# Performance work log

Hardware: AMD Instinct MI355X
Metric: run time of the kernel (lower is better)

The kernel has to match this reference:

```python
import jax, jax.numpy as jnp
import numpy as np

TEMPERATURE = 0.05   # distiller.temperature
KD_WEIGHT = 1.0      # args.kd_weight
EPS = 1e-8
B, D = 128, 768


def _huber(diff):
    a = jnp.abs(diff)
    return jnp.where(a < 1.0, 0.5 * a * a, a - 0.5)


def _pairwise_sqdist(x):
    # ||xi||^2 + ||xj||^2 - 2 xi.xj  (squared euclidean, as in source)
    n2 = (x * x).sum(axis=1, keepdims=True)
    return n2 + n2.T - 2.0 * (x @ x.T)


def _distance_loss(s, t):
    ds = _pairwise_sqdist(s)          # [N,N]
    dt = _pairwise_sqdist(t)
    n = ds.shape[0]
    mask = jnp.triu(jnp.ones((n, n), bool), k=1)
    cnt = n * (n - 1) / 2.0
    mean_sd = jax.lax.stop_gradient(jnp.where(mask, ds, 0.0).sum() / cnt) + EPS
    mean_td = jnp.where(mask, dt, 0.0).sum() / cnt + EPS  # teacher is constant anyway
    loss = _huber(ds / mean_sd - dt / mean_td)
    return jnp.where(mask, loss, 0.0).sum() / cnt


def _angle_potentials(x):
    # diffs[i,j] = x[j] - x[i]; unit vectors; cos[i,j,k] = e[i,j] . e[k,j]
    diffs = x[None, :, :] - x[:, None, :]                       # [N,N,D]
    e = diffs / (jnp.linalg.norm(diffs, axis=-1, keepdims=True) + EPS)
    return jnp.einsum('ijd,kjd->ijk', e, e)                     # [N,N,N]


def _angle_loss(s, t):
    ps = _angle_potentials(s)
    pt = _angle_potentials(t)
    n = ps.shape[0]
    i = jnp.arange(n)
    # valid iff i != j, i != k, j != k  (matches the three masked diagonals)
    m = ((i[:, None, None] != i[None, :, None]) &
         (i[:, None, None] != i[None, None, :]) &
         (i[None, :, None] != i[None, None, :]))
    cnt = n * (n - 1) * (n - 2)
    return jnp.where(m, _huber(ps - pt), 0.0).sum() / cnt


def _contrastive_loss(sq, sp):
    scores = (sq @ sp.T) / TEMPERATURE                          # [B,B]
    tgt = jnp.arange(scores.shape[0])                           # * (B//B) == arange
    logZ = jax.nn.logsumexp(scores, axis=-1)
    return (logZ - jnp.take_along_axis(scores, tgt[:, None], axis=1)[:, 0]).mean()


def setup_inputs() -> dict:
    key = jax.random.key(0)
    k1, k2, k3, k4 = jax.random.split(key, 4)
    return {
        'student_qry': jax.random.normal(k1, (B, D), jnp.float32),
        'student_pos': jax.random.normal(k2, (B, D), jnp.float32),
        'teacher_qry': jax.random.normal(k3, (B, D), jnp.float32),
        'teacher_pos': jax.random.normal(k4, (B, D), jnp.float32),
    }


def reference(student_qry, student_pos, teacher_qry, teacher_pos):
    contrastive = _contrastive_loss(student_qry, student_pos)
    s = jnp.concatenate([student_qry, student_pos], axis=0)     # [2B,D]
    t = jnp.concatenate([teacher_qry, teacher_pos], axis=0)
    t = jax.lax.stop_gradient(t)                                # teacher under no_grad
    kd = 0.5 * _distance_loss(s, t) + 0.5 * _angle_loss(s, t)
    total = contrastive + KD_WEIGHT * kd
    return total, contrastive, kd
```

## Files before the change

kernel.cpp:

```cpp
#include <hip/hip_runtime.h>
#include <math.h>

#define N2   256
#define DIM  768
#define EPSF 1e-8f

#define OFF_PART  0u
#define OFF_PDIAG 1048576u
#define OFF_GS    1052672u
#define OFF_GT    1118208u
#define OFF_INVS  1183744u
#define OFF_INVT  1249280u
#define OFF_SLOT  1314816u
#define SL_DSDT 0
#define SL_CON  512
#define SL_ANG  640
#define SL_DIST 1152

__device__ inline float wave_reduce_sum(float v) {
    #pragma unroll
    for (int o = 32; o > 0; o >>= 1) v += __shfl_down(v, o, 64);
    return v;
}
__device__ inline float wave_reduce_max(float v) {
    #pragma unroll
    for (int o = 32; o > 0; o >>= 1) v = fmaxf(v, __shfl_down(v, o, 64));
    return v;
}
__device__ inline float block_reduce_sum(float v, volatile float* red) {
    float w = wave_reduce_sum(v);
    __syncthreads();
    if ((threadIdx.x & 63) == 0) red[threadIdx.x >> 6] = w;
    __syncthreads();
    return red[0] + red[1] + red[2] + red[3];
}
__device__ inline const float* rowptr(const float* q, const float* p, int r) {
    return (r < 128) ? (q + r * DIM) : (p + (r - 128) * DIM);
}

__global__ __launch_bounds__(256) void gemm_kernel(
        const float* __restrict__ sq, const float* __restrict__ sp,
        const float* __restrict__ tq, const float* __restrict__ tp,
        float* __restrict__ ws) {
    const int b = blockIdx.x, t = threadIdx.x;
    const int c = b & 7, mat = (b >> 3) & 1, tile = b >> 4;
    const int m0 = (tile >> 2) * 64, n0 = (tile & 3) * 64;
    const float* q = mat ? tq : sq;
    const float* p = mat ? tp : sp;

    __shared__ float As[64][100];
    __shared__ float Bs[64][100];

    const int srow = t >> 2, skq = (t & 3) * 4;
    const int kb = c * 96;
    const float* arow = rowptr(q, p, m0 + srow);
    const float* brow = rowptr(q, p, n0 + srow);
    #pragma unroll
    for (int m = 0; m < 6; ++m) {
        *(float4*)&As[srow][skq + 16 * m] = *(const float4*)&arow[kb + skq + 16 * m];
        *(float4*)&Bs[srow][skq + 16 * m] = *(const float4*)&brow[kb + skq + 16 * m];
    }
    __syncthreads();

    const int ty = t >> 4, tx = t & 15;
    float acc[4][4] = {};
    for (int k = 0; k < 96; k += 4) {
        float4 av[4], bv[4];
        #pragma unroll
        for (int r = 0; r < 4; ++r) av[r] = *(const float4*)&As[ty + 16 * r][k];
        #pragma unroll
        for (int cc = 0; cc < 4; ++cc) bv[cc] = *(const float4*)&Bs[tx + 16 * cc][k];
        #pragma unroll
        for (int r = 0; r < 4; ++r) {
            const float ar4[4] = {av[r].x, av[r].y, av[r].z, av[r].w};
            #pragma unroll
            for (int cc = 0; cc < 4; ++cc) {
                const float bc4[4] = {bv[cc].x, bv[cc].y, bv[cc].z, bv[cc].w};
                acc[r][cc] = fmaf(ar4[0], bc4[0], acc[r][cc]);
                acc[r][cc] = fmaf(ar4[1], bc4[1], acc[r][cc]);
                acc[r][cc] = fmaf(ar4[2], bc4[2], acc[r][cc]);
                acc[r][cc] = fmaf(ar4[3], bc4[3], acc[r][cc]);
            }
        }
    }
    float* P = ws + OFF_PART + (unsigned)(c * 2 + mat) * 65536u;
    #pragma unroll
    for (int r = 0; r < 4; ++r) {
        const int row = m0 + ty + 16 * r;
        #pragma unroll
        for (int cc = 0; cc < 4; ++cc)
            P[row * 256 + n0 + tx + 16 * cc] = acc[r][cc];
    }
    if (m0 == n0 && ty == tx) {
        float* PD = ws + OFF_PDIAG + (unsigned)(c * 2 + mat) * 256u;
        #pragma unroll
        for (int r = 0; r < 4; ++r) PD[m0 + ty + 16 * r] = acc[r][r];
    }
}

__global__ __launch_bounds__(256) void prep_kernel(float* __restrict__ ws) {
    __shared__ float red1[4], red2[4], redS[1];
    const int b = blockIdx.x, t = threadIdx.x;

    const int mat = b >> 8, i = b & 255, j = t;
    const float* P  = ws + OFF_PART + (unsigned)mat * 65536u;
    const float* PD = ws + OFF_PDIAG + (unsigned)mat * 256u;
    float g = 0.f, dj = 0.f, di = 0.f;
    #pragma unroll
    for (int c = 0; c < 8; ++c) {
        g  += P[c * 131072 + i * 256 + j];
        dj += PD[c * 512 + j];
        di += PD[c * 512 + i];
    }
    float* G  = ws + (mat ? OFF_GT : OFF_GS);
    float* IV = ws + (mat ? OFF_INVT : OFF_INVS);
    G[i * 256 + j] = g;
    const float d = fmaxf(di + dj - 2.f * g, 0.f);
    IV[i * 256 + j] = 1.f / (sqrtf(d) + EPSF);

    const float v = block_reduce_sum((j > i) ? d : 0.f, red1);
    if (t == 0) ws[OFF_SLOT + SL_DSDT + b] = v;

    if (b < 128) {
        const float s = (j >= 128) ? 20.f * g : -INFINITY;
        if (j == 128 + i) redS[0] = s;
        float m = wave_reduce_max(s);
        __syncthreads();
        if ((t & 63) == 0) red2[t >> 6] = m;
        __syncthreads();
        const float mx = fmaxf(fmaxf(red2[0], red2[1]), fmaxf(red2[2], red2[3]));
        const float e = block_reduce_sum((j >= 128) ? expf(s - mx) : 0.f, red1);
        if (t == 0) ws[OFF_SLOT + SL_CON + b] = mx + logf(e) - redS[0];
    }
}

__global__ __launch_bounds__(256) void angle_kernel(float* __restrict__ ws) {
    const float* Gs = ws + OFF_GS;
    const float* Gt = ws + OFF_GT;
    const float* IS = ws + OFF_INVS;
    const float* IT = ws + OFF_INVT;
    __shared__ float sGJ[16][68], sIJ[16][68], sTJ[16][68], sITJ[16][68];
    __shared__ float red1[4], red2[4];
    const int b = blockIdx.x, t = threadIdx.x;

    if (b < 512) {
        const int k0 = (b & 3) * 64;
        const int j0 = ((b >> 2) & 15) * 16;
        const int i0 = (b >> 6) * 32;
        const int jj = t & 15, ii = t >> 4;
        const int i1 = i0 + ii, i2 = i1 + 16, j = j0 + jj;
        {
            const int r = t >> 4, c = (t & 15) * 4;
            const int g = (j0 + r) * N2 + k0 + c;
            *(float4*)&sGJ[r][c]  = *(const float4*)&Gs[g];
            *(float4*)&sIJ[r][c]  = *(const float4*)&IS[g];
            *(float4*)&sTJ[r][c]  = *(const float4*)&Gt[g];
            *(float4*)&sITJ[r][c] = *(const float4*)&IT[g];
        }
        const float Gjj = Gs[j * 257], Tjj = Gt[j * 257];
        const float wis1 = IS[i1 * N2 + j], wit1 = IT[i1 * N2 + j];
        const float wis2 = IS[i2 * N2 + j], wit2 = IT[i2 * N2 + j];
        const float as1 = (Gjj - Gs[i1 * N2 + j]) * wis1;
        const float at1 = (Tjj - Gt[i1 * N2 + j]) * wit1;
        const float as2 = (Gjj - Gs[i2 * N2 + j]) * wis2;
        const float at2 = (Tjj - Gt[i2 * N2 + j]) * wit2;
        const float* gI1 = Gs + i1 * N2 + k0;
        const float* tI1 = Gt + i1 * N2 + k0;
        const float* gI2 = Gs + i2 * N2 + k0;
        const float* tI2 = Gt + i2 * N2 + k0;
        __syncthreads();

        float sum1 = 0.f, sum2 = 0.f;
        for (int c = 0; c < 64; c += 4) {
            const float4 gJ  = *(const float4*)&sGJ[jj][c];
            const float4 iJ  = *(const float4*)&sIJ[jj][c];
            const float4 tJ  = *(const float4*)&sTJ[jj][c];
            const float4 itJ = *(const float4*)&sITJ[jj][c];
            const float4 a1 = *(const float4*)&gI1[c];
            const float4 b1 = *(const float4*)&tI1[c];
            const float4 a2 = *(const float4*)&gI2[c];
            const float4 b2 = *(const float4*)&tI2[c];
            const float gJr[4]  = {gJ.x, gJ.y, gJ.z, gJ.w};
            const float iJr[4]  = {iJ.x, iJ.y, iJ.z, iJ.w};
            const float tJr[4]  = {tJ.x, tJ.y, tJ.z, tJ.w};
            const float itJr[4] = {itJ.x, itJ.y, itJ.z, itJ.w};
            const float a1r[4] = {a1.x, a1.y, a1.z, a1.w};
            const float b1r[4] = {b1.x, b1.y, b1.z, b1.w};
            const float a2r[4] = {a2.x, a2.y, a2.z, a2.w};
            const float b2r[4] = {b2.x, b2.y, b2.z, b2.w};
            #pragma unroll
            for (int e = 0; e < 4; ++e) {
                const float ps1 = fmaf(wis1, a1r[e] - gJr[e], as1) * iJr[e];
                const float pt1 = fmaf(wit1, b1r[e] - tJr[e], at1) * itJr[e];
                const float d1 = ps1 - pt1;
                const float ad1 = fabsf(d1);
                const float m1 = fminf(ad1, 1.f);
                sum1 = fmaf(m1, fmaf(-0.5f, m1, ad1), sum1);

                const float ps2 = fmaf(wis2, a2r[e] - gJr[e], as2) * iJr[e];
                const float pt2 = fmaf(wit2, b2r[e] - tJr[e], at2) * itJr[e];
                const float d2 = ps2 - pt2;
                const float ad2 = fabsf(d2);
                const float m2 = fminf(ad2, 1.f);
                sum2 = fmaf(m2, fmaf(-0.5f, m2, ad2), sum2);
            }
        }
        const float v = block_reduce_sum(sum1 + sum2, red1);
        if (t == 0) ws[OFF_SLOT + SL_ANG + b] = v;
    } else {
        const float sds = block_reduce_sum(ws[OFF_SLOT + SL_DSDT + t], red1);
        const float sdt = block_reduce_sum(ws[OFF_SLOT + SL_DSDT + 256 + t], red2);
        const float rs = 1.f / (sds / 32640.f + EPSF);
        const float rt = 1.f / (sdt / 32640.f + EPSF);
        const int i = b - 512;
        const float dsv = fmaxf(Gs[i * 257] + Gs[t * 257] - 2.f * Gs[i * N2 + t], 0.f);
        const float dtv = fmaxf(Gt[i * 257] + Gt[t * 257] - 2.f * Gt[i * N2 + t], 0.f);
        const float dd = dsv * rs - dtv * rt;
        const float a = fabsf(dd);
        const float m = fminf(a, 1.f);
        const float hv = block_reduce_sum((t > i) ? m * fmaf(-0.5f, m, a) : 0.f, red1);
        if (t == 0) ws[OFF_SLOT + SL_DIST + i] = hv;
    }
}

__global__ __launch_bounds__(256) void finalize_kernel(const float* __restrict__ ws,
                                                       float* __restrict__ out) {
    __shared__ float red1[4];
    const int t = threadIdx.x;
    const float* S = ws + OFF_SLOT;
    const float c_ = block_reduce_sum((t < 128) ? S[SL_CON + t] : 0.f, red1);
    const float a_ = block_reduce_sum(S[SL_ANG + t] + S[SL_ANG + 256 + t], red1);
    const float d_ = block_reduce_sum(S[SL_DIST + t], red1);
    if (t == 0) {
        const float contrastive = c_ / 128.f;
        const float dist = d_ / 32640.f;
        const float ang = a_ / 16581120.f;
        const float kd = 0.5f * (dist + ang);
        out[0] = contrastive + kd;
        out[1] = contrastive;
        out[2] = kd;
    }
}

extern "C" void kernel_launch(void* const* d_in, const int* in_sizes, int n_in,
                              void* d_out, int out_size, void* d_ws, size_t ws_size,
                              hipStream_t stream) {
    (void)in_sizes; (void)n_in; (void)out_size; (void)ws_size;
    const float* sq = (const float*)d_in[0];
    const float* sp = (const float*)d_in[1];
    const float* tq = (const float*)d_in[2];
    const float* tp = (const float*)d_in[3];
    float* ws  = (float*)d_ws;
    float* out = (float*)d_out;

    gemm_kernel<<<256, 256, 0, stream>>>(sq, sp, tq, tp, ws);
    prep_kernel<<<512, 256, 0, stream>>>(ws);
    angle_kernel<<<768, 256, 0, stream>>>(ws);
    finalize_kernel<<<1, 256, 0, stream>>>(ws, out);
}
```

Baseline: 82.27 us.

## Fold distance loss into prep kernel and drop finalize kernel via atomics

The mean pairwise distance is now computed analytically from the Gram trace and total tile sums emitted by the GEMM kernel. That lets the distance Huber term be evaluated inside the prep kernel instead of in extra angle-kernel blocks. Final reductions switch to atomicAdd into the output, which removes the finalize kernel launch, and the prep kernel processes student and teacher together per row. The trade-offs are nondeterministic float atomic ordering and a cancellation-prone mean formula (256*trace minus the sum of all Gram entries).

```diff
diff --git a/kernel.cpp b/kernel.cpp
--- a/kernel.cpp
+++ b/kernel.cpp
@@ -7,15 +7,11 @@
 
 #define OFF_PART  0u
 #define OFF_PDIAG 1048576u
-#define OFF_GS    1052672u
-#define OFF_GT    1118208u
-#define OFF_INVS  1183744u
-#define OFF_INVT  1249280u
-#define OFF_SLOT  1314816u
-#define SL_DSDT 0
-#define SL_CON  512
-#define SL_ANG  640
-#define SL_DIST 1152
+#define OFF_TSUM  1052672u
+#define OFF_GS    1052928u
+#define OFF_GT    1118464u
+#define OFF_INVS  1184000u
+#define OFF_INVT  1249536u
 
 __device__ inline float wave_reduce_sum(float v) {
     #pragma unroll
@@ -41,8 +37,9 @@
 __global__ __launch_bounds__(256) void gemm_kernel(
         const float* __restrict__ sq, const float* __restrict__ sp,
         const float* __restrict__ tq, const float* __restrict__ tp,
-        float* __restrict__ ws) {
+        float* __restrict__ ws, float* __restrict__ out) {
     const int b = blockIdx.x, t = threadIdx.x;
+    if (b == 0 && t < 3) out[t] = 0.f;
     const int c = b & 7, mat = (b >> 3) & 1, tile = b >> 4;
     const int m0 = (tile >> 2) * 64, n0 = (tile & 3) * 64;
     const float* q = mat ? tq : sq;
@@ -50,6 +47,7 @@
 
     __shared__ float As[64][100];
     __shared__ float Bs[64][100];
+    __shared__ float redg[4];
 
     const int srow = t >> 2, skq = (t & 3) * 4;
     const int kb = c * 96;
@@ -84,161 +82,160 @@
         }
     }
     float* P = ws + OFF_PART + (unsigned)(c * 2 + mat) * 65536u;
+    float ts = 0.f;
     #pragma unroll
     for (int r = 0; r < 4; ++r) {
         const int row = m0 + ty + 16 * r;
         #pragma unroll
-        for (int cc = 0; cc < 4; ++cc)
+        for (int cc = 0; cc < 4; ++cc) {
             P[row * 256 + n0 + tx + 16 * cc] = acc[r][cc];
+            ts += acc[r][cc];
+        }
     }
     if (m0 == n0 && ty == tx) {
         float* PD = ws + OFF_PDIAG + (unsigned)(c * 2 + mat) * 256u;
         #pragma unroll
         for (int r = 0; r < 4; ++r) PD[m0 + ty + 16 * r] = acc[r][r];
     }
-}
-
-__global__ __launch_bounds__(256) void prep_kernel(float* __restrict__ ws) {
+    const float tsum = block_reduce_sum(ts, redg);
+    if (t == 0) ws[OFF_TSUM + (unsigned)(mat * 128 + c * 16 + tile)] = tsum;
+}
+
+__global__ __launch_bounds__(256) void prep_kernel(float* __restrict__ ws,
+                                                   float* __restrict__ out) {
     __shared__ float red1[4], red2[4], redS[1];
-    const int b = blockIdx.x, t = threadIdx.x;
-
-    const int mat = b >> 8, i = b & 255, j = t;
-    const float* P  = ws + OFF_PART + (unsigned)mat * 65536u;
-    const float* PD = ws + OFF_PDIAG + (unsigned)mat * 256u;
-    float g = 0.f, dj = 0.f, di = 0.f;
+    const int i = blockIdx.x, j = threadIdx.x, t = threadIdx.x;
+
+    const float* P  = ws + OFF_PART;
+    const float* PD = ws + OFF_PDIAG;
+    float gs = 0.f, gt = 0.f, djs = 0.f, djt = 0.f, dis = 0.f, dit = 0.f;
     #pragma unroll
     for (int c = 0; c < 8; ++c) {
-        g  += P[c * 131072 + i * 256 + j];
-        dj += PD[c * 512 + j];
-        di += PD[c * 512 + i];
-    }
-    float* G  = ws + (mat ? OFF_GT : OFF_GS);
-    float* IV = ws + (mat ? OFF_INVT : OFF_INVS);
-    G[i * 256 + j] = g;
-    const float d = fmaxf(di + dj - 2.f * g, 0.f);
-    IV[i * 256 + j] = 1.f / (sqrtf(d) + EPSF);
-
-    const float v = block_reduce_sum((j > i) ? d : 0.f, red1);
-    if (t == 0) ws[OFF_SLOT + SL_DSDT + b] = v;
-
-    if (b < 128) {
-        const float s = (j >= 128) ? 20.f * g : -INFINITY;
+        gs  += P[c * 131072 + i * 256 + j];
+        gt  += P[c * 131072 + 65536 + i * 256 + j];
+        djs += PD[c * 512 + j];
+        djt += PD[c * 512 + 256 + j];
+        dis += PD[c * 512 + i];
+        dit += PD[c * 512 + 256 + i];
+    }
+    (ws + OFF_GS)[i * 256 + j] = gs;
+    (ws + OFF_GT)[i * 256 + j] = gt;
+    const float ds = fmaxf(dis + djs - 2.f * gs, 0.f);
+    const float dt = fmaxf(dit + djt - 2.f * gt, 0.f);
+    (ws + OFF_INVS)[i * 256 + j] = 1.f / (sqrtf(ds) + EPSF);
+    (ws + OFF_INVT)[i * 256 + j] = 1.f / (sqrtf(dt) + EPSF);
+
+    const float tr_s = block_reduce_sum(djs, red1);
+    const float tr_t = block_reduce_sum(djt, red1);
+    const float tv = ws[OFF_TSUM + t];
+    const float sum_gs = block_reduce_sum((t < 128) ? tv : 0.f, red1);
+    const float sum_gt = block_reduce_sum((t >= 128) ? tv : 0.f, red1);
+    const float rs = 1.f / ((256.f * tr_s - sum_gs) / 32640.f + EPSF);
+    const float rt = 1.f / ((256.f * tr_t - sum_gt) / 32640.f + EPSF);
+
+    const float dd = ds * rs - dt * rt;
+    const float a = fabsf(dd);
+    const float m = fminf(a, 1.f);
+    const float hv = block_reduce_sum((j > i) ? m * fmaf(-0.5f, m, a) : 0.f, red1);
+    if (t == 0) {
+        const float c0 = 0.5f * hv / 32640.f;
+        atomicAdd(&out[0], c0);
+        atomicAdd(&out[2], c0);
+    }
+
+    if (i < 128) {
+        const float s = (j >= 128) ? 20.f * gs : -INFINITY;
         if (j == 128 + i) redS[0] = s;
-        float m = wave_reduce_max(s);
+        float mx0 = wave_reduce_max(s);
         __syncthreads();
-        if ((t & 63) == 0) red2[t >> 6] = m;
+        if ((t & 63) == 0) red2[t >> 6] = mx0;
         __syncthreads();
         const float mx = fmaxf(fmaxf(red2[0], red2[1]), fmaxf(red2[2], red2[3]));
         const float e = block_reduce_sum((j >= 128) ? expf(s - mx) : 0.f, red1);
-        if (t == 0) ws[OFF_SLOT + SL_CON + b] = mx + logf(e) - redS[0];
-    }
-}
-
-__global__ __launch_bounds__(256) void angle_kernel(float* __restrict__ ws) {
+        if (t == 0) {
+            const float cb = (mx + logf(e) - redS[0]) / 128.f;
+            atomicAdd(&out[0], cb);
+            atomicAdd(&out[1], cb);
+        }
+    }
+}
+
+__global__ __launch_bounds__(256) void angle_kernel(float* __restrict__ ws,
+                                                    float* __restrict__ out) {
     const float* Gs = ws + OFF_GS;
     const float* Gt = ws + OFF_GT;
     const float* IS = ws + OFF_INVS;
     const float* IT = ws + OFF_INVT;
     __shared__ float sGJ[16][68], sIJ[16][68], sTJ[16][68], sITJ[16][68];
-    __shared__ float red1[4], red2[4];
+    __shared__ float red1[4];
     const int b = blockIdx.x, t = threadIdx.x;
 
-    if (b < 512) {
-        const int k0 = (b & 3) * 64;
-        const int j0 = ((b >> 2) & 15) * 16;
-        const int i0 = (b >> 6) * 32;
-        const int jj = t & 15, ii = t >> 4;
-        const int i1 = i0 + ii, i2 = i1 + 16, j = j0 + jj;
-        {
-            const int r = t >> 4, c = (t & 15) * 4;
-            const int g = (j0 + r) * N2 + k0 + c;
-            *(float4*)&sGJ[r][c]  = *(const float4*)&Gs[g];
-            *(float4*)&sIJ[r][c]  = *(const float4*)&IS[g];
-            *(float4*)&sTJ[r][c]  = *(const float4*)&Gt[g];
-            *(float4*)&sITJ[r][c] = *(const float4*)&IT[g];
-        }
-        const float Gjj = Gs[j * 257], Tjj = Gt[j * 257];
-        const float wis1 = IS[i1 * N2 + j], wit1 = IT[i1 * N2 + j];
-        const float wis2 = IS[i2 * N2 + j], wit2 = IT[i2 * N2 + j];
-        const float as1 = (Gjj - Gs[i1 * N2 + j]) * wis1;
-        const float at1 = (Tjj - Gt[i1 * N2 + j]) * wit1;
-        const float as2 = (Gjj - Gs[i2 * N2 + j]) * wis2;
-        const float at2 = (Tjj - Gt[i2 * N2 + j]) * wit2;
-        const float* gI1 = Gs + i1 * N2 + k0;
-        const float* tI1 = Gt + i1 * N2 + k0;
-        const float* gI2 = Gs + i2 * N2 + k0;
-        const float* tI2 = Gt + i2 * N2 + k0;
-        __syncthreads();
-
-        float sum1 = 0.f, sum2 = 0.f;
-        for (int c = 0; c < 64; c += 4) {
-            const float4 gJ  = *(const float4*)&sGJ[jj][c];
-            const float4 iJ  = *(const float4*)&sIJ[jj][c];
-            const float4 tJ  = *(const float4*)&sTJ[jj][c];
-            const float4 itJ = *(const float4*)&sITJ[jj][c];
-            const float4 a1 = *(const float4*)&gI1[c];
-            const float4 b1 = *(const float4*)&tI1[c];
-            const float4 a2 = *(const float4*)&gI2[c];
-            const float4 b2 = *(const float4*)&tI2[c];
-            const float gJr[4]  = {gJ.x, gJ.y, gJ.z, gJ.w};
-            const float iJr[4]  = {iJ.x, iJ.y, iJ.z, iJ.w};
-            const float tJr[4]  = {tJ.x, tJ.y, tJ.z, tJ.w};
-            const float itJr[4] = {itJ.x, itJ.y, itJ.z, itJ.w};
-            const float a1r[4] = {a1.x, a1.y, a1.z, a1.w};
-            const float b1r[4] = {b1.x, b1.y, b1.z, b1.w};
-            const float a2r[4] = {a2.x, a2.y, a2.z, a2.w};
-            const float b2r[4] = {b2.x, b2.y, b2.z, b2.w};
-            #pragma unroll
-            for (int e = 0; e < 4; ++e) {
-                const float ps1 = fmaf(wis1, a1r[e] - gJr[e], as1) * iJr[e];
-                const float pt1 = fmaf(wit1, b1r[e] - tJr[e], at1) * itJr[e];
-                const float d1 = ps1 - pt1;
-                const float ad1 = fabsf(d1);
-                const float m1 = fminf(ad1, 1.f);
-                sum1 = fmaf(m1, fmaf(-0.5f, m1, ad1), sum1);
-
-                const float ps2 = fmaf(wis2, a2r[e] - gJr[e], as2) * iJr[e];
-                const float pt2 = fmaf(wit2, b2r[e] - tJr[e], at2) * itJr[e];
-                const float d2 = ps2 - pt2;
-                const float ad2 = fabsf(d2);
-                const float m2 = fminf(ad2, 1.f);
-                sum2 = fmaf(m2, fmaf(-0.5f, m2, ad2), sum2);
-            }
-        }
-        const float v = block_reduce_sum(sum1 + sum2, red1);
-        if (t == 0) ws[OFF_SLOT + SL_ANG + b] = v;
-    } else {
-        const float sds = block_reduce_sum(ws[OFF_SLOT + SL_DSDT + t], red1);
-        const float sdt = block_reduce_sum(ws[OFF_SLOT + SL_DSDT + 256 + t], red2);
-        const float rs = 1.f / (sds / 32640.f + EPSF);
-        const float rt = 1.f / (sdt / 32640.f + EPSF);
-        const int i = b - 512;
-        const float dsv = fmaxf(Gs[i * 257] + Gs[t * 257] - 2.f * Gs[i * N2 + t], 0.f);
-        const float dtv = fmaxf(Gt[i * 257] + Gt[t * 257] - 2.f * Gt[i * N2 + t], 0.f);
-        const float dd = dsv * rs - dtv * rt;
-        const float a = fabsf(dd);
-        const float m = fminf(a, 1.f);
-        const float hv = block_reduce_sum((t > i) ? m * fmaf(-0.5f, m, a) : 0.f, red1);
-        if (t == 0) ws[OFF_SLOT + SL_DIST + i] = hv;
-    }
-}
-
-__global__ __launch_bounds__(256) void finalize_kernel(const float* __restrict__ ws,
-                                                       float* __restrict__ out) {
-    __shared__ float red1[4];
-    const int t = threadIdx.x;
-    const float* S = ws + OFF_SLOT;
-    const float c_ = block_reduce_sum((t < 128) ? S[SL_CON + t] : 0.f, red1);
-    const float a_ = block_reduce_sum(S[SL_ANG + t] + S[SL_ANG + 256 + t], red1);
-    const float d_ = block_reduce_sum(S[SL_DIST + t], red1);
+    const int k0 = (b & 3) * 64;
+    const int j0 = ((b >> 2) & 15) * 16;
+    const int i0 = (b >> 6) * 32;
+    const int jj = t & 15, ii = t >> 4;
+    const int i1 = i0 + ii, i2 = i1 + 16, j = j0 + jj;
+    {
+        const int r = t >> 4, c = (t & 15) * 4;
+        const int g = (j0 + r) * N2 + k0 + c;
+        *(float4*)&sGJ[r][c]  = *(const float4*)&Gs[g];
+        *(float4*)&sIJ[r][c]  = *(const float4*)&IS[g];
+        *(float4*)&sTJ[r][c]  = *(const float4*)&Gt[g];
+        *(float4*)&sITJ[r][c] = *(const float4*)&IT[g];
+    }
+    const float Gjj = Gs[j * 257], Tjj = Gt[j * 257];
+    const float wis1 = IS[i1 * N2 + j], wit1 = IT[i1 * N2 + j];
+    const float wis2 = IS[i2 * N2 + j], wit2 = IT[i2 * N2 + j];
+    const float as1 = (Gjj - Gs[i1 * N2 + j]) * wis1;
+    const float at1 = (Tjj - Gt[i1 * N2 + j]) * wit1;
+    const float as2 = (Gjj - Gs[i2 * N2 + j]) * wis2;
+    const float at2 = (Tjj - Gt[i2 * N2 + j]) * wit2;
+    const float* gI1 = Gs + i1 * N2 + k0;
+    const float* tI1 = Gt + i1 * N2 + k0;
+    const float* gI2 = Gs + i2 * N2 + k0;
+    const float* tI2 = Gt + i2 * N2 + k0;
+    __syncthreads();
+
+    float sum1 = 0.f, sum2 = 0.f;
+    for (int c = 0; c < 64; c += 4) {
+        const float4 gJ  = *(const float4*)&sGJ[jj][c];
+        const float4 iJ  = *(const float4*)&sIJ[jj][c];
+        const float4 tJ  = *(const float4*)&sTJ[jj][c];
+        const float4 itJ = *(const float4*)&sITJ[jj][c];
+        const float4 a1 = *(const float4*)&gI1[c];
+        const float4 b1 = *(const float4*)&tI1[c];
+        const float4 a2 = *(const float4*)&gI2[c];
+        const float4 b2 = *(const float4*)&tI2[c];
+        const float gJr[4]  = {gJ.x, gJ.y, gJ.z, gJ.w};
+        const float iJr[4]  = {iJ.x, iJ.y, iJ.z, iJ.w};
+        const float tJr[4]  = {tJ.x, tJ.y, tJ.z, tJ.w};
+        const float itJr[4] = {itJ.x, itJ.y, itJ.z, itJ.w};
+        const float a1r[4] = {a1.x, a1.y, a1.z, a1.w};
+        const float b1r[4] = {b1.x, b1.y, b1.z, b1.w};
+        const float a2r[4] = {a2.x, a2.y, a2.z, a2.w};
+        const float b2r[4] = {b2.x, b2.y, b2.z, b2.w};
+        #pragma unroll
+        for (int e = 0; e < 4; ++e) {
+            const float ps1 = fmaf(wis1, a1r[e] - gJr[e], as1) * iJr[e];
+            const float pt1 = fmaf(wit1, b1r[e] - tJr[e], at1) * itJr[e];
+            const float d1 = ps1 - pt1;
+            const float ad1 = fabsf(d1);
+            const float m1 = fminf(ad1, 1.f);
+            sum1 = fmaf(m1, fmaf(-0.5f, m1, ad1), sum1);
+
+            const float ps2 = fmaf(wis2, a2r[e] - gJr[e], as2) * iJr[e];
+            const float pt2 = fmaf(wit2, b2r[e] - tJr[e], at2) * itJr[e];
+            const float d2 = ps2 - pt2;
+            const float ad2 = fabsf(d2);
+            const float m2 = fminf(ad2, 1.f);
+            sum2 = fmaf(m2, fmaf(-0.5f, m2, ad2), sum2);
+        }
+    }
+    const float v = block_reduce_sum(sum1 + sum2, red1);
     if (t == 0) {
-        const float contrastive = c_ / 128.f;
-        const float dist = d_ / 32640.f;
-        const float ang = a_ / 16581120.f;
-        const float kd = 0.5f * (dist + ang);
-        out[0] = contrastive + kd;
-        out[1] = contrastive;
-        out[2] = kd;
+        const float c0 = 0.5f * v / 16581120.f;
+        atomicAdd(&out[0], c0);
+        atomicAdd(&out[2], c0);
     }
 }
 
@@ -253,8 +250,7 @@
     float* ws  = (float*)d_ws;
     float* out = (float*)d_out;
 
-    gemm_kernel<<<256, 256, 0, stream>>>(sq, sp, tq, tp, ws);
-    prep_kernel<<<512, 256, 0, stream>>>(ws);
-    angle_kernel<<<768, 256, 0, stream>>>(ws);
-    finalize_kernel<<<1, 256, 0, stream>>>(ws, out);
-}
+    gemm_kernel<<<256, 256, 0, stream>>>(sq, sp, tq, tp, ws, out);
+    prep_kernel<<<256, 256, 0, stream>>>(ws, out);
+    angle_kernel<<<512, 256, 0, stream>>>(ws, out);
+}
```

After: 101.0 us. 22.8% more time.
